# Kernel tuning notes

Hardware: AMD Instinct MI355X
Metric: run time of the kernel (lower is better)

## Reference

```python
import jax, jax.numpy as jnp
import numpy as np

B, N, NFEAT = 32, 512, 256
NHID, NHEADS, NOUT = 64, 8, 128
ALPHA = 0.2    # GraphAttn LeakyReLU slope
ACVT_SLOPE = 0.01  # default nn.LeakyReLU slope in GAT.acvt
EPS = 1e-12


def _leaky(x, slope):
    return jnp.where(x >= 0, x, slope * x)


def setup_inputs() -> dict:
    key = jax.random.key(0)
    ks = jax.random.split(key, 10)
    s = lambda fan_in: 1.0 / np.sqrt(fan_in)
    return {
        "batch_descs": jax.random.normal(ks[0], (B, N, NFEAT), dtype=jnp.float32),
        # per-head GraphAttn params (nn.Linear weights, no bias)
        "W_tran": jax.random.uniform(ks[1], (NHEADS, NHID, NFEAT), jnp.float32, -s(NFEAT), s(NFEAT)),
        "a1": jax.random.uniform(ks[2], (NHEADS, NHID), jnp.float32, -s(NHID), s(NHID)),
        "a2": jax.random.uniform(ks[3], (NHEADS, NHID), jnp.float32, -s(NHID), s(NHID)),
        # output GraphAttn: in = NHID*NHEADS, out = NOUT
        "W_out": jax.random.uniform(ks[4], (NOUT, NHID * NHEADS), jnp.float32, -s(NHID * NHEADS), s(NHID * NHEADS)),
        "a1_out": jax.random.uniform(ks[5], (NOUT,), jnp.float32, -s(NOUT), s(NOUT)),
        "a2_out": jax.random.uniform(ks[6], (NOUT,), jnp.float32, -s(NOUT), s(NOUT)),
        # final nn.Linear(nout, nout) with bias
        "W_lin": jax.random.uniform(ks[7], (NOUT, NOUT), jnp.float32, -s(NOUT), s(NOUT)),
        "b_lin": jax.random.uniform(ks[8], (NOUT,), jnp.float32, -s(NOUT), s(NOUT)),
    }


def reference(batch_descs, W_tran, a1, a2, W_out, a1_out, a2_out, W_lin, b_lin):
    def gat_one_object(x):  # x: [N, NFEAT]; dense all-ones adj (ignored by GraphAttn)
        # ---- multi-head GraphAttn ----
        h = jnp.einsum('nf,hdf->hnd', x, W_tran)          # [H, N, NHID]
        e1 = jnp.einsum('hnd,hd->hn', h, a1)              # [H, N]
        e2 = jnp.einsum('hnd,hd->hn', h, a2)              # [H, N]
        # e[h, j, k] = a1(h_k) + a2(h_j); softmax over k (torch dim=1 on [N,N])
        e = _leaky(e1[:, None, :] + e2[:, :, None], ALPHA)  # [H, N, N]
        att = jax.nn.softmax(e, axis=-1)
        o = jnp.einsum('hjk,hkd->hjd', att, h)            # [H, N, NHID]
        o = jnp.transpose(o, (1, 0, 2)).reshape(N, NHEADS * NHID)  # concat heads
        # ---- acvt (dropout2 is identity in eval) ----
        x2 = _leaky(o, ACVT_SLOPE)
        # ---- output GraphAttn ----
        h2 = x2 @ W_out.T                                 # [N, NOUT]
        f1 = h2 @ a1_out                                  # [N]
        f2 = h2 @ a2_out                                  # [N]
        e_o = _leaky(f1[None, :] + f2[:, None], ALPHA)    # [N, N]
        att_o = jax.nn.softmax(e_o, axis=-1)
        out = att_o @ h2                                  # [N, NOUT]
        out = jnp.mean(out, axis=0)                       # [NOUT]
        return out @ W_lin.T + b_lin

    feats = jax.vmap(gat_one_object)(batch_descs)         # [B, NOUT]
    # F.normalize(p=2, dim=-1) with eps clamp
    norm = jnp.maximum(jnp.linalg.norm(feats, axis=-1, keepdims=True), EPS)
    return feats / norm
```

## Files before the change

### kernel.cpp

```cpp
#include <hip/hip_runtime.h>
#include <hip/hip_bf16.h>
#include <math.h>

#define ALPHA 0.2f
#define ACVT 0.01f

typedef __attribute__((ext_vector_type(8))) __bf16 bf16x8;
typedef __attribute__((ext_vector_type(4))) __bf16 bf16x4;
typedef __attribute__((ext_vector_type(4))) float f32x4;

__device__ __forceinline__ bf16x8 cvt8(const float* p) {
    float4 v0 = *(const float4*)p;
    float4 v1 = *(const float4*)(p + 4);
    bf16x8 o;
    o[0] = (__bf16)v0.x; o[1] = (__bf16)v0.y; o[2] = (__bf16)v0.z; o[3] = (__bf16)v0.w;
    o[4] = (__bf16)v1.x; o[5] = (__bf16)v1.y; o[6] = (__bf16)v1.z; o[7] = (__bf16)v1.w;
    return o;
}

__global__ __launch_bounds__(256) void gemm1_f(
    const float* __restrict__ X, const float* __restrict__ Wt,
    __bf16* __restrict__ HT,
    const float* __restrict__ a1, const float* __restrict__ a2,
    float* __restrict__ E1, float* __restrict__ E2) {
    __shared__ char As[128 * 128];
    __shared__ char Bs[128 * 128];
    const int tid = threadIdx.x;
    const int w = tid >> 6, lane = tid & 63;
    const int wm = w >> 1, wn = w & 1;
    const int r = lane & 15, g = lane >> 4;
    const int m0 = blockIdx.x * 128;
    const int n0 = blockIdx.y * 128;

    f32x4 acc[4][4];
#pragma unroll
    for (int mt = 0; mt < 4; ++mt)
#pragma unroll
        for (int nt = 0; nt < 4; ++nt) {
            acc[mt][nt][0] = 0.f; acc[mt][nt][1] = 0.f;
            acc[mt][nt][2] = 0.f; acc[mt][nt][3] = 0.f;
        }

    const int sr = tid >> 3;
    const int c8 = (tid & 7) * 8;

    for (int k0 = 0; k0 < 256; k0 += 64) {
        __syncthreads();
#pragma unroll
        for (int i = 0; i < 4; ++i) {
            int row = sr + i * 32;
            bf16x8 va = cvt8(X + (size_t)(m0 + row) * 256 + k0 + c8);
            *(bf16x8*)(As + row * 128 + ((c8 * 2) ^ ((row & 7) << 4))) = va;
            bf16x8 vb = cvt8(Wt + (size_t)(n0 + row) * 256 + k0 + c8);
            *(bf16x8*)(Bs + row * 128 + ((c8 * 2) ^ ((row & 7) << 4))) = vb;
        }
        __syncthreads();
#pragma unroll
        for (int kk = 0; kk < 64; kk += 32) {
            bf16x8 af[4], bfv[4];
#pragma unroll
            for (int mt = 0; mt < 4; ++mt) {
                int row = wm * 64 + mt * 16 + r;
                af[mt] = *(const bf16x8*)(As + row * 128 +
                                          (((kk + g * 8) * 2) ^ ((row & 7) << 4)));
            }
#pragma unroll
            for (int nt = 0; nt < 4; ++nt) {
                int row = wn * 64 + nt * 16 + r;
                bfv[nt] = *(const bf16x8*)(Bs + row * 128 +
                                           (((kk + g * 8) * 2) ^ ((row & 7) << 4)));
            }
#pragma unroll
            for (int mt = 0; mt < 4; ++mt)
#pragma unroll
                for (int nt = 0; nt < 4; ++nt)
                    acc[mt][nt] = __builtin_amdgcn_mfma_f32_16x16x32_bf16(
                        af[mt], bfv[nt], acc[mt][nt], 0, 0, 0);
        }
    }

    const int h = blockIdx.y * 2 + wn;
#pragma unroll
    for (int mt = 0; mt < 4; ++mt) {
        int mfirst = m0 + wm * 64 + mt * 16 + g * 4;
        int b = mfirst >> 9, nn = mfirst & 511;
#pragma unroll
        for (int nt = 0; nt < 4; ++nt) {
            int d = nt * 16 + r;
            bf16x4 pv;
#pragma unroll
            for (int reg = 0; reg < 4; ++reg) pv[reg] = (__bf16)acc[mt][nt][reg];
            *(bf16x4*)(HT + ((size_t)(b * 8 + h) * 64 + d) * 512 + nn) = pv;
        }
    }
    float w1[4], w2[4];
#pragma unroll
    for (int nt = 0; nt < 4; ++nt) {
        w1[nt] = a1[h * 64 + nt * 16 + r];
        w2[nt] = a2[h * 64 + nt * 16 + r];
    }
#pragma unroll
    for (int mt = 0; mt < 4; ++mt)
#pragma unroll
        for (int reg = 0; reg < 4; ++reg) {
            float s1 = 0.f, s2 = 0.f;
#pragma unroll
            for (int nt = 0; nt < 4; ++nt) {
                s1 += acc[mt][nt][reg] * w1[nt];
                s2 += acc[mt][nt][reg] * w2[nt];
            }
#pragma unroll
            for (int off = 1; off <= 8; off <<= 1) {
                s1 += __shfl_xor(s1, off, 64);
                s2 += __shfl_xor(s2, off, 64);
            }
            if (r == 0) {
                int m = m0 + wm * 64 + mt * 16 + g * 4 + reg;
                int b = m >> 9, n = m & 511;
                E1[(size_t)(b * 8 + h) * 512 + n] = s1;
                E2[(size_t)(b * 8 + h) * 512 + n] = s2;
            }
        }
}

__global__ __launch_bounds__(256) void attn_g(const __bf16* __restrict__ HT,
                                              const float* __restrict__ E1,
                                              const float* __restrict__ E2,
                                              __bf16* __restrict__ OL) {
    __shared__ float e1s[512];
    __shared__ float red[4][64];
    __shared__ float e1maxS;

    const int bid = blockIdx.x;
    const int bh = bid >> 1, half = bid & 1;
    const int b = bh >> 3, h = bh & 7;
    const int tid = threadIdx.x;
    const int w = tid >> 6, lane = tid & 63;
    const int r = lane & 15, g = lane >> 4;

    for (int i = tid; i < 512; i += 256) e1s[i] = E1[(size_t)bh * 512 + i];
    __syncthreads();

    ((float*)red)[tid] = fmaxf(e1s[tid], e1s[tid + 256]);
    __syncthreads();
    if (tid < 64) {
        const float* rp = (const float*)red;
        float m = fmaxf(fmaxf(rp[tid], rp[tid + 64]), fmaxf(rp[tid + 128], rp[tid + 192]));
#pragma unroll
        for (int off = 32; off >= 1; off >>= 1) m = fmaxf(m, __shfl_xor(m, off, 64));
        if (tid == 0) e1maxS = m;
    }
    __syncthreads();
    const float e1max = e1maxS;

    float ee2[4], mm[4];
    const float* e2g = E2 + (size_t)bh * 512 + half * 256 + w * 64;
#pragma unroll
    for (int mt = 0; mt < 4; ++mt) {
        float v = e2g[mt * 16 + r];
        ee2[mt] = v;
        float s = e1max + v;
        mm[mt] = fmaxf(s, ALPHA * s);
    }

    f32x4 acc[4][4];
#pragma unroll
    for (int mt = 0; mt < 4; ++mt)
#pragma unroll
        for (int nt = 0; nt < 4; ++nt) {
            acc[mt][nt][0] = 0.f; acc[mt][nt][1] = 0.f;
            acc[mt][nt][2] = 0.f; acc[mt][nt][3] = 0.f;
        }
    float zac[4] = {0.f, 0.f, 0.f, 0.f};

    const __bf16* hb = HT + (size_t)bh * 32768;
    bf16x8 cur[4], nxt[4];
#pragma unroll
    for (int nt = 0; nt < 4; ++nt)
        cur[nt] = *(const bf16x8*)(hb + (size_t)(nt * 16 + r) * 512 + g * 8);

    for (int c = 0; c < 16; ++c) {
        if (c < 15) {
#pragma unroll
            for (int nt = 0; nt < 4; ++nt)
                nxt[nt] = *(const bf16x8*)(hb + (size_t)(nt * 16 + r) * 512 +
                                           (c + 1) * 32 + g * 8);
        }
        const float* ep = e1s + c * 32 + g * 8;
        float4 ea = *(const float4*)(ep);
        float4 eb = *(const float4*)(ep + 4);
        float e1c[8] = {ea.x, ea.y, ea.z, ea.w, eb.x, eb.y, eb.z, eb.w};

#pragma unroll
        for (int mt = 0; mt < 4; ++mt) {
            bf16x8 af;
            float zp = 0.f;
#pragma unroll
            for (int q = 0; q < 8; ++q) {
                float s = e1c[q] + ee2[mt];
                s = fmaxf(s, ALPHA * s);
                float p = __expf(s - mm[mt]);
                zp += p;
                af[q] = (__bf16)p;
            }
            zac[mt] += zp;
#pragma unroll
            for (int nt = 0; nt < 4; ++nt)
                acc[mt][nt] =
                    __builtin_amdgcn_mfma_f32_16x16x32_bf16(af, cur[nt], acc[mt][nt], 0, 0, 0);
        }
        if (c < 15) {
#pragma unroll
            for (int nt = 0; nt < 4; ++nt) cur[nt] = nxt[nt];
        }
    }

#pragma unroll
    for (int mt = 0; mt < 4; ++mt) {
        float z = zac[mt];
        z += __shfl_xor(z, 16, 64);
        z += __shfl_xor(z, 32, 64);
        if (g == 0) red[w][mt * 16 + r] = 1.f / z;
    }

    __bf16* ob = OL + ((size_t)b * 512 + half * 256 + w * 64) * 512 + h * 64;
#pragma unroll
    for (int mt = 0; mt < 4; ++mt) {
#pragma unroll
        for (int reg = 0; reg < 4; ++reg) {
            int row = mt * 16 + g * 4 + reg;
            float zi = red[w][row];
#pragma unroll
            for (int nt = 0; nt < 4; ++nt) {
                float v = acc[mt][nt][reg] * zi;
                v = fmaxf(v, ACVT * v);
                ob[(size_t)row * 512 + nt * 16 + r] = (__bf16)v;
            }
        }
    }
}

__global__ __launch_bounds__(256) void gemm2_f(
    const __bf16* __restrict__ OL, const float* __restrict__ Wo,
    float* __restrict__ H2,
    const float* __restrict__ a1o, const float* __restrict__ a2o,
    float* __restrict__ F1, float* __restrict__ F2) {
    __shared__ char As[32 * 128];
    __shared__ char Bs[128 * 128];
    __shared__ float fred[2][32][2];
    const int tid = threadIdx.x;
    const int w = tid >> 6, lane = tid & 63;
    const int wm = w >> 1, wn = w & 1;
    const int r = lane & 15, g = lane >> 4;
    const int m0 = blockIdx.x * 32;

    f32x4 acc[4];
#pragma unroll
    for (int nt = 0; nt < 4; ++nt) {
        acc[nt][0] = 0.f; acc[nt][1] = 0.f; acc[nt][2] = 0.f; acc[nt][3] = 0.f;
    }

    const int sra = tid >> 3;
    const int c8 = (tid & 7) * 8;

    for (int k0 = 0; k0 < 512; k0 += 64) {
        __syncthreads();
        {
            bf16x8 va = *(const bf16x8*)((const char*)OL +
                                         ((size_t)(m0 + sra) * 512 + k0) * 2 + c8 * 2);
            *(bf16x8*)(As + sra * 128 + ((c8 * 2) ^ ((sra & 7) << 4))) = va;
        }
#pragma unroll
        for (int i = 0; i < 4; ++i) {
            int row = sra + i * 32;
            bf16x8 vb = cvt8(Wo + (size_t)row * 512 + k0 + c8);
            *(bf16x8*)(Bs + row * 128 + ((c8 * 2) ^ ((row & 7) << 4))) = vb;
        }
        __syncthreads();
#pragma unroll
        for (int kk = 0; kk < 64; kk += 32) {
            int arow = wm * 16 + r;
            bf16x8 af = *(const bf16x8*)(As + arow * 128 +
                                         (((kk + g * 8) * 2) ^ ((arow & 7) << 4)));
            bf16x8 bfv[4];
#pragma unroll
            for (int nt = 0; nt < 4; ++nt) {
                int row = wn * 64 + nt * 16 + r;
                bfv[nt] = *(const bf16x8*)(Bs + row * 128 +
                                           (((kk + g * 8) * 2) ^ ((row & 7) << 4)));
            }
#pragma unroll
            for (int nt = 0; nt < 4; ++nt)
                acc[nt] = __builtin_amdgcn_mfma_f32_16x16x32_bf16(af, bfv[nt], acc[nt], 0, 0, 0);
        }
    }

#pragma unroll
    for (int reg = 0; reg < 4; ++reg) {
        int row = m0 + wm * 16 + g * 4 + reg;
#pragma unroll
        for (int nt = 0; nt < 4; ++nt)
            H2[(size_t)row * 128 + wn * 64 + nt * 16 + r] = acc[nt][reg];
    }
    float w1[4], w2[4];
#pragma unroll
    for (int nt = 0; nt < 4; ++nt) {
        w1[nt] = a1o[wn * 64 + nt * 16 + r];
        w2[nt] = a2o[wn * 64 + nt * 16 + r];
    }
#pragma unroll
    for (int reg = 0; reg < 4; ++reg) {
        float s1 = 0.f, s2 = 0.f;
#pragma unroll
        for (int nt = 0; nt < 4; ++nt) {
            s1 += acc[nt][reg] * w1[nt];
            s2 += acc[nt][reg] * w2[nt];
        }
#pragma unroll
        for (int off = 1; off <= 8; off <<= 1) {
            s1 += __shfl_xor(s1, off, 64);
            s2 += __shfl_xor(s2, off, 64);
        }
        if (r == 0) {
            int lr = wm * 16 + g * 4 + reg;
            fred[wn][lr][0] = s1;
            fred[wn][lr][1] = s2;
        }
    }
    __syncthreads();
    if (tid < 32) {
        int m = m0 + tid;
        int b = m >> 9, n = m & 511;
        F1[(size_t)b * 512 + n] = fred[0][tid][0] + fred[1][tid][0];
        F2[(size_t)b * 512 + n] = fred[0][tid][1] + fred[1][tid][1];
    }
}

__global__ __launch_bounds__(256) void zw_k(const float* __restrict__ F1,
                                            const float* __restrict__ F2,
                                            float* __restrict__ WP) {
    __shared__ float f1s[512];
    __shared__ float wpart[4][512];
    __shared__ float redm[256];
    const int b = blockIdx.x >> 4, jc = blockIdx.x & 15;
    const int tid = threadIdx.x;
    const int w = tid >> 6, lane = tid & 63;

    f1s[tid] = F1[(size_t)b * 512 + tid];
    f1s[tid + 256] = F1[(size_t)b * 512 + tid + 256];
#pragma unroll
    for (int i = 0; i < 8; ++i) wpart[w][lane + 64 * i] = 0.f;
    __syncthreads();
    redm[tid] = fmaxf(f1s[tid], f1s[tid + 256]);
    __syncthreads();
    if (tid < 64) {
        float m = fmaxf(fmaxf(redm[tid], redm[tid + 64]), fmaxf(redm[tid + 128], redm[tid + 192]));
#pragma unroll
        for (int off = 32; off >= 1; off >>= 1) m = fmaxf(m, __shfl_xor(m, off, 64));
        if (tid == 0) redm[0] = m;
    }
    __syncthreads();
    const float f1m = redm[0];

    for (int jj = 0; jj < 8; ++jj) {
        int j = jc * 32 + w * 8 + jj;
        float f2j = F2[(size_t)b * 512 + j];
        float sj = f1m + f2j;
        float mj = fmaxf(sj, ALPHA * sj);
        float pv[8];
        float z = 0.f;
#pragma unroll
        for (int i = 0; i < 8; ++i) {
            float s = f1s[lane + 64 * i] + f2j;
            s = fmaxf(s, ALPHA * s);
            float p = __expf(s - mj);
            pv[i] = p;
            z += p;
        }
#pragma unroll
        for (int off = 32; off >= 1; off >>= 1) z += __shfl_xor(z, off, 64);
        float inv = 1.f / z;
#pragma unroll
        for (int i = 0; i < 8; ++i) wpart[w][lane + 64 * i] += pv[i] * inv;
    }
    __syncthreads();
    for (int i = tid; i < 512; i += 256)
        WP[(size_t)(b * 16 + jc) * 512 + i] =
            wpart[0][i] + wpart[1][i] + wpart[2][i] + wpart[3][i];
}

__global__ __launch_bounds__(512) void finalv_k(const float* __restrict__ WP,
                                                const float* __restrict__ H2,
                                                const float* __restrict__ Wl,
                                                const float* __restrict__ bl,
                                                float* __restrict__ out) {
    __shared__ float wsL[512];
    __shared__ float part[4][128];
    __shared__ float vs[128];
    __shared__ float fo_s[128];
    __shared__ float r0;
    const int b = blockIdx.x, tid = threadIdx.x;
    {
        float s = 0.f;
#pragma unroll
        for (int jc = 0; jc < 16; ++jc) s += WP[(size_t)(b * 16 + jc) * 512 + tid];
        wsL[tid] = s;
    }
    __syncthreads();
    {
        const int q = tid >> 7, d = tid & 127;
        const float* h2p = H2 + ((size_t)b * 512 + q * 128) * 128 + d;
        float acc = 0.f;
#pragma unroll 8
        for (int i = 0; i < 128; ++i) acc += wsL[q * 128 + i] * h2p[(size_t)i * 128];
        part[q][d] = acc;
    }
    __syncthreads();
    if (tid < 128)
        vs[tid] = (part[0][tid] + part[1][tid] + part[2][tid] + part[3][tid]) * (1.f / 512.f);
    __syncthreads();
    if (tid < 128) {
        float fo = bl[tid];
        const float* wl = Wl + (size_t)tid * 128;
#pragma unroll 4
        for (int d = 0; d < 128; d += 4)
            fo += vs[d] * wl[d] + vs[d + 1] * wl[d + 1] + vs[d + 2] * wl[d + 2] +
                  vs[d + 3] * wl[d + 3];
        fo_s[tid] = fo;
    }
    __syncthreads();
    if (tid < 64) {
        float s = fo_s[tid] * fo_s[tid] + fo_s[tid + 64] * fo_s[tid + 64];
#pragma unroll
        for (int off = 32; off >= 1; off >>= 1) s += __shfl_xor(s, off, 64);
        if (tid == 0) r0 = s;
    }
    __syncthreads();
    float inv = 1.f / fmaxf(sqrtf(r0), 1e-12f);
    if (tid < 128) out[(size_t)b * 128 + tid] = fo_s[tid] * inv;
}

extern "C" void kernel_launch(void* const* d_in, const int* in_sizes, int n_in,
                              void* d_out, int out_size, void* d_ws, size_t ws_size,
                              hipStream_t stream) {
    const float* X = (const float*)d_in[0];
    const float* Wt = (const float*)d_in[1];
    const float* a1 = (const float*)d_in[2];
    const float* a2 = (const float*)d_in[3];
    const float* Wo = (const float*)d_in[4];
    const float* a1o = (const float*)d_in[5];
    const float* a2o = (const float*)d_in[6];
    const float* Wl = (const float*)d_in[7];
    const float* bl = (const float*)d_in[8];
    float* out = (float*)d_out;

    char* p = (char*)d_ws;
    __bf16* HT = (__bf16*)p;  p += (size_t)8388608 * 2;
    __bf16* OL = (__bf16*)p;  p += (size_t)8388608 * 2;
    float* E1 = (float*)p;    p += (size_t)131072 * 4;
    float* E2 = (float*)p;    p += (size_t)131072 * 4;
    float* H2 = (float*)p;    p += (size_t)2097152 * 4;
    float* F1 = (float*)p;    p += (size_t)16384 * 4;
    float* F2 = (float*)p;    p += (size_t)16384 * 4;
    float* WP = (float*)p;    p += (size_t)262144 * 4;

    gemm1_f<<<dim3(128, 4), 256, 0, stream>>>(X, Wt, HT, a1, a2, E1, E2);
    attn_g<<<512, 256, 0, stream>>>(HT, E1, E2, OL);
    gemm2_f<<<512, 256, 0, stream>>>(OL, Wo, H2, a1o, a2o, F1, F2);
    zw_k<<<512, 256, 0, stream>>>(F1, F2, WP);
    finalv_k<<<32, 512, 0, stream>>>(WP, H2, Wl, bl, out);
}
```

Measured before the change: 146.3 us.

## Stage HT stores via LDS, split attention into quarters with shared H tiles, bf16 H2

gemm1 now writes its HT output through an LDS transpose buffer so global stores are contiguous 16-byte rows, and it remaps block IDs so blocks are scheduled in a different order. The attention kernel moves from 2 to 4 blocks per batch-head, giving 1024 blocks with 32 rows per wave. Each block stages the H chunk into swizzled LDS and shares it across waves, instead of every wave loading its own copy from global. H2 is now stored in bf16 to halve its traffic into finalv. In exchange this adds barriers per chunk in attention, duplicates the E1 max reduction across more blocks, and lowers H2 precision.

```diff
diff --git a/kernel.cpp b/kernel.cpp
--- a/kernel.cpp
+++ b/kernel.cpp
@@ -25,12 +25,16 @@
     float* __restrict__ E1, float* __restrict__ E2) {
     __shared__ char As[128 * 128];
     __shared__ char Bs[128 * 128];
+    __shared__ char Tt[128 * 264];
     const int tid = threadIdx.x;
     const int w = tid >> 6, lane = tid & 63;
     const int wm = w >> 1, wn = w & 1;
     const int r = lane & 15, g = lane >> 4;
-    const int m0 = blockIdx.x * 128;
-    const int n0 = blockIdx.y * 128;
+    const int L = blockIdx.x;
+    const int W = (L & 7) * 64 + (L >> 3);
+    const int m_tile = W >> 2, n_tile = W & 3;
+    const int m0 = m_tile * 128;
+    const int n0 = n_tile * 128;
 
     f32x4 acc[4][4];
 #pragma unroll
@@ -79,20 +83,31 @@
         }
     }
 
-    const int h = blockIdx.y * 2 + wn;
 #pragma unroll
     for (int mt = 0; mt < 4; ++mt) {
-        int mfirst = m0 + wm * 64 + mt * 16 + g * 4;
-        int b = mfirst >> 9, nn = mfirst & 511;
+        int node = wm * 64 + mt * 16 + g * 4;
 #pragma unroll
         for (int nt = 0; nt < 4; ++nt) {
-            int d = nt * 16 + r;
+            int d_blk = wn * 64 + nt * 16 + r;
             bf16x4 pv;
 #pragma unroll
             for (int reg = 0; reg < 4; ++reg) pv[reg] = (__bf16)acc[mt][nt][reg];
-            *(bf16x4*)(HT + ((size_t)(b * 8 + h) * 64 + d) * 512 + nn) = pv;
-        }
-    }
+            *(bf16x4*)(Tt + d_blk * 264 + node * 2) = pv;
+        }
+    }
+    __syncthreads();
+    {
+        const int b = m0 >> 9, nn = m0 & 511;
+        const int h0 = n_tile * 2;
+#pragma unroll
+        for (int i = 0; i < 8; ++i) {
+            int d_row = (tid >> 4) + i * 16;
+            int hrow = (b * 8 + h0 + (d_row >> 6)) * 64 + (d_row & 63);
+            bf16x8 v = *(const bf16x8*)(Tt + d_row * 264 + (tid & 15) * 16);
+            *(bf16x8*)(HT + (size_t)hrow * 512 + nn + (tid & 15) * 8) = v;
+        }
+    }
+    const int h = n_tile * 2 + wn;
     float w1[4], w2[4];
 #pragma unroll
     for (int nt = 0; nt < 4; ++nt) {
@@ -123,16 +138,18 @@
         }
 }
 
-__global__ __launch_bounds__(256) void attn_g(const __bf16* __restrict__ HT,
+__global__ __launch_bounds__(256) void attn_s(const __bf16* __restrict__ HT,
                                               const float* __restrict__ E1,
                                               const float* __restrict__ E2,
                                               __bf16* __restrict__ OL) {
+    __shared__ char Hc[4096];
     __shared__ float e1s[512];
-    __shared__ float red[4][64];
+    __shared__ float redm[256];
+    __shared__ float zrow[4][32];
     __shared__ float e1maxS;
 
     const int bid = blockIdx.x;
-    const int bh = bid >> 1, half = bid & 1;
+    const int bh = bid >> 2, qq = bid & 3;
     const int b = bh >> 3, h = bh & 7;
     const int tid = threadIdx.x;
     const int w = tid >> 6, lane = tid & 63;
@@ -140,12 +157,11 @@
 
     for (int i = tid; i < 512; i += 256) e1s[i] = E1[(size_t)bh * 512 + i];
     __syncthreads();
-
-    ((float*)red)[tid] = fmaxf(e1s[tid], e1s[tid + 256]);
+    redm[tid] = fmaxf(e1s[tid], e1s[tid + 256]);
     __syncthreads();
     if (tid < 64) {
-        const float* rp = (const float*)red;
-        float m = fmaxf(fmaxf(rp[tid], rp[tid + 64]), fmaxf(rp[tid + 128], rp[tid + 192]));
+        float m = fmaxf(fmaxf(redm[tid], redm[tid + 64]),
+                        fmaxf(redm[tid + 128], redm[tid + 192]));
 #pragma unroll
         for (int off = 32; off >= 1; off >>= 1) m = fmaxf(m, __shfl_xor(m, off, 64));
         if (tid == 0) e1maxS = m;
@@ -153,46 +169,50 @@
     __syncthreads();
     const float e1max = e1maxS;
 
-    float ee2[4], mm[4];
-    const float* e2g = E2 + (size_t)bh * 512 + half * 256 + w * 64;
-#pragma unroll
-    for (int mt = 0; mt < 4; ++mt) {
+    float ee2[2], mm[2];
+    const float* e2g = E2 + (size_t)bh * 512 + qq * 128 + w * 32;
+#pragma unroll
+    for (int mt = 0; mt < 2; ++mt) {
         float v = e2g[mt * 16 + r];
         ee2[mt] = v;
         float s = e1max + v;
         mm[mt] = fmaxf(s, ALPHA * s);
     }
 
-    f32x4 acc[4][4];
-#pragma unroll
-    for (int mt = 0; mt < 4; ++mt)
+    f32x4 acc[2][4];
+#pragma unroll
+    for (int mt = 0; mt < 2; ++mt)
 #pragma unroll
         for (int nt = 0; nt < 4; ++nt) {
             acc[mt][nt][0] = 0.f; acc[mt][nt][1] = 0.f;
             acc[mt][nt][2] = 0.f; acc[mt][nt][3] = 0.f;
         }
-    float zac[4] = {0.f, 0.f, 0.f, 0.f};
-
-    const __bf16* hb = HT + (size_t)bh * 32768;
-    bf16x8 cur[4], nxt[4];
-#pragma unroll
-    for (int nt = 0; nt < 4; ++nt)
-        cur[nt] = *(const bf16x8*)(hb + (size_t)(nt * 16 + r) * 512 + g * 8);
+    float zac[2] = {0.f, 0.f};
+
+    const int d_s = tid >> 2, kq = tid & 3;
+    const __bf16* hsrc = HT + (size_t)(bh * 64 + d_s) * 512 + kq * 8;
+    const int lw = d_s * 64 + ((kq * 16) ^ ((d_s & 3) << 4));
+    bf16x8 stg = *(const bf16x8*)hsrc;
 
     for (int c = 0; c < 16; ++c) {
-        if (c < 15) {
-#pragma unroll
-            for (int nt = 0; nt < 4; ++nt)
-                nxt[nt] = *(const bf16x8*)(hb + (size_t)(nt * 16 + r) * 512 +
-                                           (c + 1) * 32 + g * 8);
-        }
+        __syncthreads();
+        *(bf16x8*)(Hc + lw) = stg;
+        __syncthreads();
+        if (c < 15) stg = *(const bf16x8*)(hsrc + (c + 1) * 32);
+
         const float* ep = e1s + c * 32 + g * 8;
         float4 ea = *(const float4*)(ep);
         float4 eb = *(const float4*)(ep + 4);
         float e1c[8] = {ea.x, ea.y, ea.z, ea.w, eb.x, eb.y, eb.z, eb.w};
 
-#pragma unroll
-        for (int mt = 0; mt < 4; ++mt) {
+        bf16x8 bfr[4];
+#pragma unroll
+        for (int nt = 0; nt < 4; ++nt) {
+            int d = nt * 16 + r;
+            bfr[nt] = *(const bf16x8*)(Hc + d * 64 + ((g * 16) ^ ((d & 3) << 4)));
+        }
+#pragma unroll
+        for (int mt = 0; mt < 2; ++mt) {
             bf16x8 af;
             float zp = 0.f;
 #pragma unroll
@@ -207,29 +227,25 @@
 #pragma unroll
             for (int nt = 0; nt < 4; ++nt)
                 acc[mt][nt] =
-                    __builtin_amdgcn_mfma_f32_16x16x32_bf16(af, cur[nt], acc[mt][nt], 0, 0, 0);
-        }
-        if (c < 15) {
-#pragma unroll
-            for (int nt = 0; nt < 4; ++nt) cur[nt] = nxt[nt];
-        }
-    }
-
-#pragma unroll
-    for (int mt = 0; mt < 4; ++mt) {
+                    __builtin_amdgcn_mfma_f32_16x16x32_bf16(af, bfr[nt], acc[mt][nt], 0, 0, 0);
+        }
+    }
+
+#pragma unroll
+    for (int mt = 0; mt < 2; ++mt) {
         float z = zac[mt];
         z += __shfl_xor(z, 16, 64);
         z += __shfl_xor(z, 32, 64);
-        if (g == 0) red[w][mt * 16 + r] = 1.f / z;
-    }
-
-    __bf16* ob = OL + ((size_t)b * 512 + half * 256 + w * 64) * 512 + h * 64;
-#pragma unroll
-    for (int mt = 0; mt < 4; ++mt) {
+        if (g == 0) zrow[w][mt * 16 + r] = 1.f / z;
+    }
+
+    __bf16* ob = OL + ((size_t)b * 512 + qq * 128 + w * 32) * 512 + h * 64;
+#pragma unroll
+    for (int mt = 0; mt < 2; ++mt) {
 #pragma unroll
         for (int reg = 0; reg < 4; ++reg) {
             int row = mt * 16 + g * 4 + reg;
-            float zi = red[w][row];
+            float zi = zrow[w][row];
 #pragma unroll
             for (int nt = 0; nt < 4; ++nt) {
                 float v = acc[mt][nt][reg] * zi;
@@ -242,7 +258,7 @@
 
 __global__ __launch_bounds__(256) void gemm2_f(
     const __bf16* __restrict__ OL, const float* __restrict__ Wo,
-    float* __restrict__ H2,
+    __bf16* __restrict__ H2,
     const float* __restrict__ a1o, const float* __restrict__ a2o,
     float* __restrict__ F1, float* __restrict__ F2) {
     __shared__ char As[32 * 128];
@@ -300,7 +316,7 @@
         int row = m0 + wm * 16 + g * 4 + reg;
 #pragma unroll
         for (int nt = 0; nt < 4; ++nt)
-            H2[(size_t)row * 128 + wn * 64 + nt * 16 + r] = acc[nt][reg];
+            H2[(size_t)row * 128 + wn * 64 + nt * 16 + r] = (__bf16)acc[nt][reg];
     }
     float w1[4], w2[4];
 #pragma unroll
@@ -390,7 +406,7 @@
 }
 
 __global__ __launch_bounds__(512) void finalv_k(const float* __restrict__ WP,
-                                                const float* __restrict__ H2,
+                                                const __bf16* __restrict__ H2,
                                                 const float* __restrict__ Wl,
                                                 const float* __restrict__ bl,
                                                 float* __restrict__ out) {
@@ -409,10 +425,10 @@
     __syncthreads();
     {
         const int q = tid >> 7, d = tid & 127;
-        const float* h2p = H2 + ((size_t)b * 512 + q * 128) * 128 + d;
+        const __bf16* h2p = H2 + ((size_t)b * 512 + q * 128) * 128 + d;
         float acc = 0.f;
 #pragma unroll 8
-        for (int i = 0; i < 128; ++i) acc += wsL[q * 128 + i] * h2p[(size_t)i * 128];
+        for (int i = 0; i < 128; ++i) acc += wsL[q * 128 + i] * (float)h2p[(size_t)i * 128];
         part[q][d] = acc;
     }
     __syncthreads();
@@ -459,13 +475,13 @@
     __bf16* OL = (__bf16*)p;  p += (size_t)8388608 * 2;
     float* E1 = (float*)p;    p += (size_t)131072 * 4;
     float* E2 = (float*)p;    p += (size_t)131072 * 4;
-    float* H2 = (float*)p;    p += (size_t)2097152 * 4;
+    __bf16* H2 = (__bf16*)p;  p += (size_t)2097152 * 2;
     float* F1 = (float*)p;    p += (size_t)16384 * 4;
     float* F2 = (float*)p;    p += (size_t)16384 * 4;
     float* WP = (float*)p;    p += (size_t)262144 * 4;
 
-    gemm1_f<<<dim3(128, 4), 256, 0, stream>>>(X, Wt, HT, a1, a2, E1, E2);
-    attn_g<<<512, 256, 0, stream>>>(HT, E1, E2, OL);
+    gemm1_f<<<512, 256, 0, stream>>>(X, Wt, HT, a1, a2, E1, E2);
+    attn_s<<<1024, 256, 0, stream>>>(HT, E1, E2, OL);
     gemm2_f<<<512, 256, 0, stream>>>(OL, Wo, H2, a1o, a2o, F1, F2);
     zw_k<<<512, 256, 0, stream>>>(F1, F2, WP);
     finalv_k<<<32, 512, 0, stream>>>(WP, H2, Wl, bl, out);
```

Result: no change. 143.6 us (-1.8%).
